# Optimization experiments

Hardware: AMD Instinct MI355X
Metric: run time of the kernel (lower is better)

## Reference

```python
import jax, jax.numpy as jnp
import numpy as np

NEG = -1e9

def gat_layer(x, edge_mask, W, al, ar, rW, b, act):
    # x: (B, N, Fin); edge_mask: (B, N, N) bool, edge u->v at [b,u,v]
    B, N, _ = x.shape
    H, D = al.shape
    f = (x @ W).reshape(B, N, H, D)                      # (B,N,H,D)
    el = jnp.einsum('bnhd,hd->bnh', f, al)               # src term
    er = jnp.einsum('bnhd,hd->bnh', f, ar)               # dst term
    # e[b,u,v,h] = LeakyReLU(el[src=u] + er[dst=v]), slope 0.2 (dgl default)
    e = jax.nn.leaky_relu(el[:, :, None, :] + er[:, None, :, :], 0.2)
    logits = jnp.where(edge_mask[..., None], e, NEG)
    # masked, empty-column-safe softmax over incoming edges (axis=1 = src u)
    m = jnp.max(logits, axis=1, keepdims=True)
    p = jnp.exp(logits - m) * edge_mask[..., None]
    alpha = p / jnp.clip(jnp.sum(p, axis=1, keepdims=True), 1e-9)
    out = jnp.einsum('buvh,buhd->bvhd', alpha, f)        # scatter-sum to dst
    res = (x @ rW).reshape(B, N, H, D)                   # residual projection
    out = out + res + b.reshape(H, D)
    return act(out) if act is not None else out


def setup_inputs() -> dict:
    key = jax.random.key(0)
    ks = jax.random.split(key, 12)
    n, c, h, w = 16, 64, 32, 32
    num_s, hid, H = 64, 64, 4
    seg = jax.random.normal(ks[0], (n, c, h, w), dtype=jnp.float32)
    adj = jax.random.normal(ks[1], (n, h * w, h * w), dtype=jnp.float32)
    s = 0.1
    return {
        'seg': seg, 'adj': adj,
        'W0': jax.random.normal(ks[2], (num_s, H * hid), dtype=jnp.float32) * s,
        'al0': jax.random.normal(ks[3], (H, hid), dtype=jnp.float32) * s,
        'ar0': jax.random.normal(ks[4], (H, hid), dtype=jnp.float32) * s,
        'rW0': jax.random.normal(ks[5], (num_s, H * hid), dtype=jnp.float32) * s,
        'b0': jnp.zeros((H * hid,), dtype=jnp.float32),
        'W1': jax.random.normal(ks[6], (H * hid, H * num_s), dtype=jnp.float32) * s,
        'al1': jax.random.normal(ks[7], (H, num_s), dtype=jnp.float32) * s,
        'ar1': jax.random.normal(ks[8], (H, num_s), dtype=jnp.float32) * s,
        'rW1': jax.random.normal(ks[9], (H * hid, H * num_s), dtype=jnp.float32) * s,
        'b1': jnp.zeros((H * num_s,), dtype=jnp.float32),
    }


def reference(seg, adj, W0, al0, ar0, rW0, b0, W1, al1, ar1, rW1, b1):
    n, c, h, w = seg.shape
    num_s = W0.shape[0]
    x = seg.reshape(n, -1, num_s)                        # (n, N, num_s)
    k = (h * w) // 6
    topv, _ = jax.lax.top_k(adj, k)
    thr = topv[..., -1]                                  # k-th largest per row
    adj_t = jnp.where(adj >= thr[..., None], adj, 0.0)
    edge_mask = adj_t > 0                                # (n, N, N)
    fea = gat_layer(x, edge_mask, W0, al0, ar0, rW0, b0, jax.nn.elu)
    fea = fea.reshape(n, fea.shape[1], -1)               # flatten heads
    fea = gat_layer(fea, edge_mask, W1, al1, ar1, rW1, b1, None)
    out = fea.mean(axis=2)                               # mean over heads -> (n, N, num_s)
    return out.reshape(n, -1, num_s)
```

## Files before the change

kernel.cpp:

```cpp
#include <hip/hip_runtime.h>
#include <hip/hip_bf16.h>
#include <stdint.h>

#define BB   16
#define NN   1024
#define KSEL 170
#define LOG2E 1.4426950408889634f

typedef __attribute__((ext_vector_type(8))) short short8;
typedef __attribute__((ext_vector_type(4))) short short4v;
typedef __attribute__((ext_vector_type(4))) float f32x4;
typedef __attribute__((ext_vector_type(2))) float float2v;

static __device__ __forceinline__ short f2bf(float x) {
    __hip_bfloat16 h = __float2bfloat16(x);
    return *reinterpret_cast<short*>(&h);
}
static __device__ __forceinline__ float bf2f(short x) {
    uint32_t u = ((uint32_t)(uint16_t)x) << 16;
    return __uint_as_float(u);
}
static __device__ __forceinline__ float fast_exp2(float x) {
    float r; asm("v_exp_f32 %0, %1" : "=v"(r) : "v"(x)); return r;
}

__global__ __launch_bounds__(256) void k_topk_mask(
    const float* __restrict__ adj, uint64_t* __restrict__ mask,
    const float* __restrict__ W0, const float* __restrict__ rW0,
    const float* __restrict__ W1, const float* __restrict__ rW1,
    const float* __restrict__ seg,
    short* __restrict__ Wt0, short* __restrict__ rWt0,
    short* __restrict__ Wt1, short* __restrict__ rWt1,
    short* __restrict__ xb0)
{
    const int bid = blockIdx.x, t = threadIdx.x;
    if (bid >= 4096) {
        const int pid = bid - 4096;
        if (pid < 64) {
            int idx = pid * 256 + t;
            int o = idx >> 6, k = idx & 63;
            Wt0[idx] = f2bf(W0[(size_t)k * 256 + o]);
        } else if (pid < 128) {
            int idx = (pid - 64) * 256 + t;
            int o = idx >> 6, k = idx & 63;
            rWt0[idx] = f2bf(rW0[(size_t)k * 256 + o]);
        } else if (pid < 384) {
            int idx = (pid - 128) * 256 + t;
            int o = idx >> 8, k = idx & 255;
            Wt1[idx] = f2bf(W1[(size_t)k * 256 + o]);
        } else if (pid < 640) {
            int idx = (pid - 384) * 256 + t;
            int o = idx >> 8, k = idx & 255;
            rWt1[idx] = f2bf(rW1[(size_t)k * 256 + o]);
        } else {
            int i = ((pid - 640) * 256 + t) * 4;
            float4 v = *(const float4*)(seg + i);
            short4v o4;
            o4[0] = f2bf(v.x); o4[1] = f2bf(v.y); o4[2] = f2bf(v.z); o4[3] = f2bf(v.w);
            *(short4v*)(xb0 + i) = o4;
        }
        return;
    }

    const int wid = t >> 6, lane = t & 63;
    const int row = bid * 4 + wid;
    const float* a = adj + (size_t)row * NN;
    __shared__ uint32_t hist[4][256];
    uint32_t* h = hist[wid];

    uint32_t key[16];
    #pragma unroll
    for (int j = 0; j < 16; ++j) {
        uint32_t u = __float_as_uint(a[lane + j * 64]);
        key[j] = u ^ ((u >> 31) ? 0xFFFFFFFFu : 0x80000000u);
    }

    uint32_t prefix = 0u, kk = KSEL;
    #pragma unroll
    for (int pass = 0; pass < 2; ++pass) {
        const int shift = 24 - 8 * pass;
        const uint32_t hi_mask = pass ? 0xFF000000u : 0u;
        *(uint4*)&h[lane * 4] = make_uint4(0u, 0u, 0u, 0u);
        __builtin_amdgcn_wave_barrier();
        #pragma unroll
        for (int j = 0; j < 16; ++j)
            if ((key[j] & hi_mask) == prefix)
                atomicAdd(&h[(key[j] >> shift) & 255], 1u);
        __builtin_amdgcn_wave_barrier();
        const uint4 c4 = *(const uint4*)&h[lane * 4];
        const uint32_t T = c4.x + c4.y + c4.z + c4.w;
        uint32_t s = T;
        #pragma unroll
        for (int off = 1; off < 64; off <<= 1) {
            uint32_t v = __shfl_down(s, off);
            s += (lane + off < 64) ? v : 0u;
        }
        const uint32_t E = s - T;
        const uint32_t s3 = c4.w;
        const uint32_t s2 = c4.z + s3;
        const uint32_t s1 = c4.y + s2;
        const uint32_t s0 = c4.x + s1;
        const uint32_t ci[4] = {c4.x, c4.y, c4.z, c4.w};
        const uint32_t si[4] = {s0, s1, s2, s3};
        uint32_t found = 0u, nb = 0u, nk = 0u;
        #pragma unroll
        for (int i = 0; i < 4; ++i) {
            uint32_t incl = E + si[i];
            uint32_t excl = incl - ci[i];
            if (excl < kk && kk <= incl) { found = 1u; nb = (uint32_t)(lane * 4 + i); nk = kk - excl; }
        }
        uint64_t bal = __ballot(found != 0u);
        int wl = __ffsll((unsigned long long)bal) - 1;
        prefix = prefix | ((uint32_t)__shfl((int)nb, wl) << shift);
        kk = (uint32_t)__shfl((int)nk, wl);
    }

    uint32_t sv[16];
    #pragma unroll
    for (int j = 0; j < 16; ++j)
        sv[j] = ((key[j] ^ prefix) >> 16) == 0u ? key[j] : 0u;

    uint32_t thr_key;
    for (;;) {
        uint32_t m = 0u;
        #pragma unroll
        for (int j = 0; j < 16; ++j) m = m > sv[j] ? m : sv[j];
        #pragma unroll
        for (int off = 1; off < 64; off <<= 1) {
            uint32_t v = __shfl_xor(m, off);
            m = m > v ? m : v;
        }
        if (m == 0u) { thr_key = 0u; break; }
        uint32_t c = 0u;
        #pragma unroll
        for (int j = 0; j < 16; ++j) c += (sv[j] == m) ? 1u : 0u;
        #pragma unroll
        for (int off = 1; off < 64; off <<= 1)
            c += __shfl_xor(c, off);
        if (kk <= c) { thr_key = m; break; }
        kk -= c;
        #pragma unroll
        for (int j = 0; j < 16; ++j) if (sv[j] == m) sv[j] = 0u;
    }

    #pragma unroll
    for (int j = 0; j < 16; ++j) {
        bool pred = (key[j] >= thr_key) && (key[j] > 0x80000000u);
        uint64_t bal = __ballot(pred);
        if (lane == 0) mask[(size_t)row * 16 + j] = bal;
    }
}

__global__ __launch_bounds__(256) void k_maskT(
    const uint64_t* __restrict__ mask, uint64_t* __restrict__ maskT)
{
    const int tile = blockIdx.x * 4 + (threadIdx.x >> 6);
    const int lane = threadIdx.x & 63;
    const int b  = tile >> 8;
    const int uw = (tile >> 4) & 15;
    const int vw = tile & 15;
    const size_t bN = (size_t)b * NN;
    uint64_t w = mask[(bN + uw * 64 + lane) * 16 + vw];
    uint64_t r_out = 0;
    #pragma unroll
    for (int j = 0; j < 64; ++j) {
        uint64_t r = __ballot((w >> j) & 1ull);
        if (lane == j) r_out = r;
    }
    maskT[(bN + vw * 64 + lane) * 16 + uw] = r_out;
}

template<int K>
__global__ __launch_bounds__(256, 2) void k_features_mfma(
    const short* __restrict__ xb,
    const short* __restrict__ Wt,
    const short* __restrict__ rWt,
    const float* __restrict__ al,
    const float* __restrict__ ar,
    short* __restrict__ ft,
    short* __restrict__ fea,
    float* __restrict__ el_t,
    float* __restrict__ er_t)
{
    const int tid = threadIdx.x, lane = tid & 63, hh = tid >> 6;
    const int l15 = lane & 15, l4 = lane >> 4;
    const int n0 = blockIdx.x * 32;
    const int b_idx = n0 >> 10;
    const int nloc = n0 & (NN - 1);
    const int bh = b_idx * 4 + hh;
    const int XP = K + 8;

    __shared__ short x_lds[32 * (K + 8)];

    const int CH = K / 8;
    #pragma unroll
    for (int c = tid; c < 32 * CH; c += 256) {
        const int row = c / CH, col = c - row * CH;
        *(short8*)&x_lds[row * XP + col * 8] =
            *(const short8*)(xb + ((size_t)n0 + row) * K + col * 8);
    }
    __syncthreads();

    const short* wbase = Wt  + (size_t)(hh * 64 + l15) * K + l4 * 8;
    const short* rbase = rWt + (size_t)(hh * 64 + l15) * K + l4 * 8;
    const size_t qs = (size_t)16 * K;

    f32x4 accf[2][4], accr[2][4];
    #pragma unroll
    for (int s = 0; s < 2; ++s)
        #pragma unroll
        for (int q = 0; q < 4; ++q) {
            accf[s][q] = (f32x4){0.f, 0.f, 0.f, 0.f};
            accr[s][q] = (f32x4){0.f, 0.f, 0.f, 0.f};
        }

    short8 bufW[2][4], bufR[2][4];
    #pragma unroll
    for (int q = 0; q < 4; ++q) {
        bufW[0][q] = *(const short8*)(wbase + q * qs);
        bufR[0][q] = *(const short8*)(rbase + q * qs);
    }

    #pragma unroll
    for (int ks = 0; ks < K / 32; ++ks) {
        const int cur = ks & 1, nxt = cur ^ 1;
        if (ks + 1 < K / 32) {
            #pragma unroll
            for (int q = 0; q < 4; ++q) {
                bufW[nxt][q] = *(const short8*)(wbase + q * qs + (ks + 1) * 32);
                bufR[nxt][q] = *(const short8*)(rbase + q * qs + (ks + 1) * 32);
            }
            __builtin_amdgcn_sched_barrier(0);
        }
        short8 x0 = *(const short8*)&x_lds[l15 * XP + ks * 32 + l4 * 8];
        short8 x1 = *(const short8*)&x_lds[(16 + l15) * XP + ks * 32 + l4 * 8];
        #pragma unroll
        for (int q = 0; q < 4; ++q) {
            accf[0][q] = __builtin_amdgcn_mfma_f32_16x16x32_bf16(x0, bufW[cur][q], accf[0][q], 0, 0, 0);
            accf[1][q] = __builtin_amdgcn_mfma_f32_16x16x32_bf16(x1, bufW[cur][q], accf[1][q], 0, 0, 0);
            accr[0][q] = __builtin_amdgcn_mfma_f32_16x16x32_bf16(bufR[cur][q], x0, accr[0][q], 0, 0, 0);
            accr[1][q] = __builtin_amdgcn_mfma_f32_16x16x32_bf16(bufR[cur][q], x1, accr[1][q], 0, 0, 0);
        }
    }

    #pragma unroll
    for (int s = 0; s < 2; ++s) {
        const int nl = nloc + s * 16;
        #pragma unroll
        for (int q = 0; q < 4; ++q) {
            short4v pk;
            #pragma unroll
            for (int r = 0; r < 4; ++r) pk[r] = f2bf(accf[s][q][r]);
            const int dl = q * 16 + l15;
            const size_t idx = ((size_t)bh << 16)
                             + (size_t)(nl >> 6) * 4096
                             + (size_t)(((nl & 63) >> 3) + (l4 >> 1)) * 512
                             + (size_t)dl * 8 + (l4 & 1) * 4;
            *(short4v*)(ft + idx) = pk;
        }
        float elv[4] = {0.f, 0.f, 0.f, 0.f}, erv[4] = {0.f, 0.f, 0.f, 0.f};
        #pragma unroll
        for (int q = 0; q < 4; ++q) {
            const float alv = al[hh * 64 + q * 16 + l15];
            const float arv = ar[hh * 64 + q * 16 + l15];
            #pragma unroll
            for (int r = 0; r < 4; ++r) {
                elv[r] = fmaf(accf[s][q][r], alv, elv[r]);
                erv[r] = fmaf(accf[s][q][r], arv, erv[r]);
            }
        }
        #pragma unroll
        for (int r = 0; r < 4; ++r) {
            #pragma unroll
            for (int off = 1; off < 16; off <<= 1) {
                elv[r] += __shfl_xor(elv[r], off);
                erv[r] += __shfl_xor(erv[r], off);
            }
        }
        if (l15 == 0) {
            float4 e4, r4;
            e4.x = elv[0] * LOG2E; e4.y = elv[1] * LOG2E;
            e4.z = elv[2] * LOG2E; e4.w = elv[3] * LOG2E;
            r4.x = erv[0] * LOG2E; r4.y = erv[1] * LOG2E;
            r4.z = erv[2] * LOG2E; r4.w = erv[3] * LOG2E;
            *(float4*)(el_t + (size_t)bh * NN + nl + l4 * 4) = e4;
            *(float4*)(er_t + (size_t)bh * NN + nl + l4 * 4) = r4;
        }
        #pragma unroll
        for (int q = 0; q < 4; ++q) {
            short4v pk;
            #pragma unroll
            for (int r = 0; r < 4; ++r) pk[r] = f2bf(accr[s][q][r]);
            *(short4v*)(fea + ((size_t)n0 + s * 16 + l15) * 256 + hh * 64 + q * 16 + l4 * 4) = pk;
        }
    }
}

template<int ELU_ON>
__global__ __launch_bounds__(256, 4) void k_attn(
    const short* __restrict__ ft,
    const float* __restrict__ el_t,
    const float* __restrict__ er_t,
    const uint64_t* __restrict__ maskT,
    const float* __restrict__ bias,
    short* fea)
{
    const int id = blockIdx.x;
    const int swz = (id & 7) * 128 + (id >> 3);
    const int b  = swz >> 6;
    const int h  = (swz >> 4) & 3;
    const int vt = swz & 15;
    const int tid = threadIdx.x;
    const int lane = tid & 63, wid = tid >> 6;
    const int l15 = lane & 15, l4 = lane >> 4;
    const int bh = b * 4 + h;
    const size_t bN = (size_t)b * NN;
    const int v0 = vt * 64;

    __shared__ __align__(16) short f_lds[3][4096];
    __shared__ __align__(16) float el_lds[NN];
    __shared__ __align__(16) uint64_t m_lds[64 * 17];
    __shared__ float smax[4];

    const short* gsrc = ft + ((size_t)bh << 16);

    {
        short8 sa = *(const short8*)(gsrc + tid * 8);
        short8 sb = *(const short8*)(gsrc + 2048 + tid * 8);
        float4 ev4 = ((const float4*)(el_t + (size_t)bh * NN))[tid];
        ((float4*)el_lds)[tid] = ev4;
        float m = fmaxf(fmaxf(ev4.x, ev4.y), fmaxf(ev4.z, ev4.w));
        #pragma unroll
        for (int off = 32; off; off >>= 1) m = fmaxf(m, __shfl_xor(m, off));
        if (lane == 0) smax[wid] = m;
        #pragma unroll
        for (int i = 0; i < 4; ++i) {
            int idx = tid + i * 256;
            m_lds[(idx >> 4) * 17 + (idx & 15)] =
                maskT[(bN + v0 + (idx >> 4)) * 16 + (idx & 15)];
        }
        *(short8*)&f_lds[0][tid * 8] = sa;
        *(short8*)&f_lds[0][2048 + tid * 8] = sb;
    }

    short8 Aa = *(const short8*)(gsrc + 4096 + tid * 8);
    short8 Ab = *(const short8*)(gsrc + 4096 + 2048 + tid * 8);

    const int vlo = wid * 16 + l15;
    const float er_lo = er_t[(size_t)bh * NN + v0 + vlo];

    __syncthreads();

    const float emx = fmaxf(fmaxf(smax[0], smax[1]), fmaxf(smax[2], smax[3]));
    const float e0 = emx + er_lo;
    const float cv_lo = fmaxf(e0, 0.2f * e0);
    const float c1_lo = er_lo - cv_lo, c2_lo = 0.2f * er_lo - cv_lo;
    const float2v c1s = {c1_lo, c1_lo};
    const float2v c2s = {c2_lo, c2_lo};
    const float2v k02 = {0.2f, 0.2f};

    const uint8_t* mbytes = (const uint8_t*)m_lds;
    const int moff_lo = vlo * 136;

    short8 ones8;
    #pragma unroll
    for (int i = 0; i < 8; ++i) ones8[i] = (short)0x3F80;

    f32x4 accLo[4];
    #pragma unroll
    for (int i = 0; i < 4; ++i) accLo[i] = (f32x4){0.f, 0.f, 0.f, 0.f};
    f32x4 dLo = (f32x4){0.f, 0.f, 0.f, 0.f};

    auto compute = [&](const short* fb, int tt) {
        #pragma unroll
        for (int kc = 0; kc < 2; ++kc) {
            const float2v* ep2 = (const float2v*)&el_lds[tt * 64 + kc * 32 + l4 * 8];
            uint32_t mLo = mbytes[moff_lo + tt * 8 + kc * 4 + l4];
            short8 aLo;
            #pragma unroll
            for (int jj = 0; jj < 4; ++jj) {
                float2v e2 = ep2[jj];
                float2v arg = __builtin_elementwise_max(e2 + c1s, e2 * k02 + c2s);
                float p0 = ((mLo >> (2 * jj)) & 1u)     ? fast_exp2(arg.x) : 0.f;
                float p1 = ((mLo >> (2 * jj + 1)) & 1u) ? fast_exp2(arg.y) : 0.f;
                aLo[2 * jj]     = f2bf(p0);
                aLo[2 * jj + 1] = f2bf(p1);
            }
            const int fo = (kc * 4 + l4) * 512 + l15 * 8;
            short8 bw0 = *(const short8*)(fb + fo);
            short8 bw1 = *(const short8*)(fb + fo + 128);
            short8 bw2 = *(const short8*)(fb + fo + 256);
            short8 bw3 = *(const short8*)(fb + fo + 384);
            __builtin_amdgcn_s_setprio(1);
            accLo[0] = __builtin_amdgcn_mfma_f32_16x16x32_bf16(aLo, bw0, accLo[0], 0, 0, 0);
            accLo[1] = __builtin_amdgcn_mfma_f32_16x16x32_bf16(aLo, bw1, accLo[1], 0, 0, 0);
            accLo[2] = __builtin_amdgcn_mfma_f32_16x16x32_bf16(aLo, bw2, accLo[2], 0, 0, 0);
            accLo[3] = __builtin_amdgcn_mfma_f32_16x16x32_bf16(aLo, bw3, accLo[3], 0, 0, 0);
            dLo      = __builtin_amdgcn_mfma_f32_16x16x32_bf16(aLo, ones8, dLo, 0, 0, 0);
            __builtin_amdgcn_s_setprio(0);
        }
    };

    short8 Ba, Bb;
    #pragma unroll 1
    for (int tt = 0; tt < 16; tt += 2) {
        if (tt + 2 < 16) {
            Ba = *(const short8*)(gsrc + (tt + 2) * 4096 + tid * 8);
            Bb = *(const short8*)(gsrc + (tt + 2) * 4096 + 2048 + tid * 8);
            __builtin_amdgcn_sched_barrier(0);
        }
        compute(f_lds[tt % 3], tt);
        {
            short* dst = f_lds[(tt + 1) % 3];
            *(short8*)&dst[tid * 8] = Aa;
            *(short8*)&dst[2048 + tid * 8] = Ab;
        }
        __syncthreads();
        if (tt + 3 < 16) {
            Aa = *(const short8*)(gsrc + (tt + 3) * 4096 + tid * 8);
            Ab = *(const short8*)(gsrc + (tt + 3) * 4096 + 2048 + tid * 8);
            __builtin_amdgcn_sched_barrier(0);
        }
        compute(f_lds[(tt + 1) % 3], tt + 1);
        if (tt + 2 < 16) {
            short* dst = f_lds[(tt + 2) % 3];
            *(short8*)&dst[tid * 8] = Ba;
            *(short8*)&dst[2048 + tid * 8] = Bb;
            __syncthreads();
        }
    }

    float rcpLo[4];
    #pragma unroll
    for (int r = 0; r < 4; ++r)
        rcpLo[r] = 1.f / fmaxf(dLo[r], 1e-9f);
    #pragma unroll
    for (int dt = 0; dt < 4; ++dt) {
        const int d = dt * 16 + l15;
        const float bv = bias[h * 64 + d];
        #pragma unroll
        for (int r = 0; r < 4; ++r) {
            const int vl = v0 + wid * 16 + l4 * 4 + r;
            const size_t rowL = (bN + vl) * 256 + h * 64 + d;
            float ov = accLo[dt][r] * rcpLo[r] + bf2f(fea[rowL]) + bv;
            if (ELU_ON) ov = ov > 0.f ? ov : __expf(ov) - 1.f;
            fea[rowL] = f2bf(ov);
        }
    }
}

__global__ __launch_bounds__(256) void k_headmean(
    const short* __restrict__ fea, float* __restrict__ outp)
{
    const int i = (blockIdx.x * 256 + threadIdx.x) * 8;
    const int d0 = i & 63;
    const size_t node = (size_t)(i >> 6);
    const short* p = fea + node * 256 + d0;
    short8 h0 = *(const short8*)(p);
    short8 h1 = *(const short8*)(p + 64);
    short8 h2 = *(const short8*)(p + 128);
    short8 h3 = *(const short8*)(p + 192);
    float4 o0, o1;
    #pragma unroll
    for (int j = 0; j < 4; ++j) {
        float v = 0.25f * (bf2f(h0[j]) + bf2f(h1[j]) + bf2f(h2[j]) + bf2f(h3[j]));
        (&o0.x)[j] = v;
    }
    #pragma unroll
    for (int j = 0; j < 4; ++j) {
        float v = 0.25f * (bf2f(h0[4 + j]) + bf2f(h1[4 + j]) + bf2f(h2[4 + j]) + bf2f(h3[4 + j]));
        (&o1.x)[j] = v;
    }
    *(float4*)(outp + i) = o0;
    *(float4*)(outp + i + 4) = o1;
}

extern "C" void kernel_launch(void* const* d_in, const int* in_sizes, int n_in,
                              void* d_out, int out_size, void* d_ws, size_t ws_size,
                              hipStream_t stream) {
    const float* seg = (const float*)d_in[0];
    const float* adj = (const float*)d_in[1];
    const float* W0  = (const float*)d_in[2];
    const float* al0 = (const float*)d_in[3];
    const float* ar0 = (const float*)d_in[4];
    const float* rW0 = (const float*)d_in[5];
    const float* b0  = (const float*)d_in[6];
    const float* W1  = (const float*)d_in[7];
    const float* al1 = (const float*)d_in[8];
    const float* ar1 = (const float*)d_in[9];
    const float* rW1 = (const float*)d_in[10];
    const float* b1  = (const float*)d_in[11];
    float* out = (float*)d_out;

    char* ws = (char*)d_ws;
    size_t off = 0;
    uint64_t* mask  = (uint64_t*)ws;
    off += (size_t)BB * NN * 16 * 8;
    uint64_t* maskT = (uint64_t*)(ws + off); off += (size_t)BB * NN * 16 * 8;
    short* ftb = (short*)(ws + off); off += (size_t)BB * 256 * NN * 2;
    short* fea = (short*)(ws + off); off += (size_t)BB * NN * 256 * 2;
    short* xb0 = (short*)(ws + off); off += (size_t)BB * NN * 64 * 2;
    short* Wt0  = (short*)(ws + off); off += 256 * 64 * 2;
    short* rWt0 = (short*)(ws + off); off += 256 * 64 * 2;
    short* Wt1  = (short*)(ws + off); off += 256 * 256 * 2;
    short* rWt1 = (short*)(ws + off); off += 256 * 256 * 2;
    char* r0 = (char*)mask;
    float* el   = (float*)r0;                 r0 += (size_t)BB * 4 * NN * 4;
    float* er   = (float*)r0;                 r0 += (size_t)BB * 4 * NN * 4;

    k_topk_mask<<<4096 + 1664, 256, 0, stream>>>(adj, mask, W0, rW0, W1, rW1, seg,
                                                 Wt0, rWt0, Wt1, rWt1, xb0);
    k_maskT<<<1024, 256, 0, stream>>>(mask, maskT);

    k_features_mfma<64><<<BB * NN / 32, 256, 0, stream>>>(xb0, Wt0, rWt0, al0, ar0,
                                                          ftb, fea, el, er);
    k_attn<1><<<1024, 256, 0, stream>>>(ftb, el, er, maskT, b0, fea);
    k_features_mfma<256><<<BB * NN / 32, 256, 0, stream>>>(fea, Wt1, rWt1, al1, ar1,
                                                           ftb, fea, el, er);
    k_attn<0><<<1024, 256, 0, stream>>>(ftb, el, er, maskT, b1, fea);

    k_headmean<<<BB * NN * 64 / 2048, 256, 0, stream>>>(fea, out);
}
```

Before: 150.3 us.

## Fuse mask transpose into first feature kernel and split top-k histograms

The separate mask-transpose kernel is removed. Its work now runs as extra blocks appended to the first feature-projection launch, which saves one kernel launch and lets the transpose overlap with the projection GEMM. Because the transpose now runs concurrently with that GEMM, el/er get their own workspace instead of aliasing the mask buffer. Separately, the top-k radix histogram is split into four sub-histograms per wave, one per 16-lane group, to reduce LDS atomic contention, at the cost of four times the histogram LDS and extra clear and reduce work.

```diff
diff --git a/kernel.cpp b/kernel.cpp
--- a/kernel.cpp
+++ b/kernel.cpp
@@ -65,8 +65,9 @@
     const int wid = t >> 6, lane = t & 63;
     const int row = bid * 4 + wid;
     const float* a = adj + (size_t)row * NN;
-    __shared__ uint32_t hist[4][256];
-    uint32_t* h = hist[wid];
+    __shared__ uint32_t hist[4][4][256];
+    uint32_t* h = &hist[wid][0][0];
+    uint32_t* hs = &hist[wid][lane >> 4][0];
 
     uint32_t key[16];
     #pragma unroll
@@ -80,14 +81,24 @@
     for (int pass = 0; pass < 2; ++pass) {
         const int shift = 24 - 8 * pass;
         const uint32_t hi_mask = pass ? 0xFF000000u : 0u;
-        *(uint4*)&h[lane * 4] = make_uint4(0u, 0u, 0u, 0u);
+        #pragma unroll
+        for (int s4 = 0; s4 < 4; ++s4)
+            *(uint4*)&h[s4 * 256 + lane * 4] = make_uint4(0u, 0u, 0u, 0u);
         __builtin_amdgcn_wave_barrier();
         #pragma unroll
         for (int j = 0; j < 16; ++j)
             if ((key[j] & hi_mask) == prefix)
-                atomicAdd(&h[(key[j] >> shift) & 255], 1u);
+                atomicAdd(&hs[(key[j] >> shift) & 255], 1u);
         __builtin_amdgcn_wave_barrier();
-        const uint4 c4 = *(const uint4*)&h[lane * 4];
+        uint4 c0 = *(const uint4*)&h[lane * 4];
+        uint4 c1 = *(const uint4*)&h[256 + lane * 4];
+        uint4 c2 = *(const uint4*)&h[512 + lane * 4];
+        uint4 c3 = *(const uint4*)&h[768 + lane * 4];
+        uint4 c4;
+        c4.x = c0.x + c1.x + c2.x + c3.x;
+        c4.y = c0.y + c1.y + c2.y + c3.y;
+        c4.z = c0.z + c1.z + c2.z + c3.z;
+        c4.w = c0.w + c1.w + c2.w + c3.w;
         const uint32_t T = c4.x + c4.y + c4.z + c4.w;
         uint32_t s = T;
         #pragma unroll
@@ -149,25 +160,6 @@
         uint64_t bal = __ballot(pred);
         if (lane == 0) mask[(size_t)row * 16 + j] = bal;
     }
-}
-
-__global__ __launch_bounds__(256) void k_maskT(
-    const uint64_t* __restrict__ mask, uint64_t* __restrict__ maskT)
-{
-    const int tile = blockIdx.x * 4 + (threadIdx.x >> 6);
-    const int lane = threadIdx.x & 63;
-    const int b  = tile >> 8;
-    const int uw = (tile >> 4) & 15;
-    const int vw = tile & 15;
-    const size_t bN = (size_t)b * NN;
-    uint64_t w = mask[(bN + uw * 64 + lane) * 16 + vw];
-    uint64_t r_out = 0;
-    #pragma unroll
-    for (int j = 0; j < 64; ++j) {
-        uint64_t r = __ballot((w >> j) & 1ull);
-        if (lane == j) r_out = r;
-    }
-    maskT[(bN + vw * 64 + lane) * 16 + uw] = r_out;
 }
 
 template<int K>
@@ -180,11 +172,32 @@
     short* __restrict__ ft,
     short* __restrict__ fea,
     float* __restrict__ el_t,
-    float* __restrict__ er_t)
+    float* __restrict__ er_t,
+    const uint64_t* __restrict__ mask, uint64_t* __restrict__ maskT, int nfeat)
 {
-    const int tid = threadIdx.x, lane = tid & 63, hh = tid >> 6;
+    const int bid = blockIdx.x;
+    const int tid = threadIdx.x;
+    if (bid >= nfeat) {
+        const int tile = (bid - nfeat) * 4 + (tid >> 6);
+        const int lane = tid & 63;
+        const int b  = tile >> 8;
+        const int uw = (tile >> 4) & 15;
+        const int vw = tile & 15;
+        const size_t bN = (size_t)b * NN;
+        uint64_t w = mask[(bN + uw * 64 + lane) * 16 + vw];
+        uint64_t r_out = 0;
+        #pragma unroll
+        for (int j = 0; j < 64; ++j) {
+            uint64_t r = __ballot((w >> j) & 1ull);
+            if (lane == j) r_out = r;
+        }
+        maskT[(bN + vw * 64 + lane) * 16 + uw] = r_out;
+        return;
+    }
+
+    const int lane = tid & 63, hh = tid >> 6;
     const int l15 = lane & 15, l4 = lane >> 4;
-    const int n0 = blockIdx.x * 32;
+    const int n0 = bid * 32;
     const int b_idx = n0 >> 10;
     const int nloc = n0 & (NN - 1);
     const int bh = b_idx * 4 + hh;
@@ -504,19 +517,19 @@
     short* rWt0 = (short*)(ws + off); off += 256 * 64 * 2;
     short* Wt1  = (short*)(ws + off); off += 256 * 256 * 2;
     short* rWt1 = (short*)(ws + off); off += 256 * 256 * 2;
-    char* r0 = (char*)mask;
-    float* el   = (float*)r0;                 r0 += (size_t)BB * 4 * NN * 4;
-    float* er   = (float*)r0;                 r0 += (size_t)BB * 4 * NN * 4;
+    float* el   = (float*)(ws + off); off += (size_t)BB * 4 * NN * 4;
+    float* er   = (float*)(ws + off); off += (size_t)BB * 4 * NN * 4;
 
     k_topk_mask<<<4096 + 1664, 256, 0, stream>>>(adj, mask, W0, rW0, W1, rW1, seg,
                                                  Wt0, rWt0, Wt1, rWt1, xb0);
-    k_maskT<<<1024, 256, 0, stream>>>(mask, maskT);
-
-    k_features_mfma<64><<<BB * NN / 32, 256, 0, stream>>>(xb0, Wt0, rWt0, al0, ar0,
-                                                          ftb, fea, el, er);
+
+    k_features_mfma<64><<<512 + 1024, 256, 0, stream>>>(xb0, Wt0, rWt0, al0, ar0,
+                                                        ftb, fea, el, er,
+                                                        mask, maskT, 512);
     k_attn<1><<<1024, 256, 0, stream>>>(ftb, el, er, maskT, b0, fea);
-    k_features_mfma<256><<<BB * NN / 32, 256, 0, stream>>>(fea, Wt1, rWt1, al1, ar1,
-                                                           ftb, fea, el, er);
+    k_features_mfma<256><<<512, 256, 0, stream>>>(fea, Wt1, rWt1, al1, ar1,
+                                                  ftb, fea, el, er,
+                                                  mask, maskT, 512);
     k_attn<0><<<1024, 256, 0, stream>>>(ftb, el, er, maskT, b1, fea);
 
     k_headmean<<<BB * NN * 64 / 2048, 256, 0, stream>>>(fea, out);
```

After: 148.6 us. Within noise of the previous version (-1.1%).
